# Kernel tuning notes

Measured on AMD Instinct MI355X. Metric: run time of the kernel, lower is better.

Reference implementation:

```python
import jax, jax.numpy as jnp
import numpy as np

N_K = 20000; N_E = 50000; N_U = 100000; EMB = 128
E_UND = 200000; E_EK = 400000; E_EU = 600000


def _gat(h, W, a, src, dst, n):
    """RCD GraphLayer: single-head GAT with edge softmax over incoming edges."""
    z = h @ W                                  # [N, d]
    d = z.shape[1]
    el = z @ a[:d]                             # src contribution to attn logit
    er = z @ a[d:]                             # dst contribution
    e = jax.nn.leaky_relu(el[src] + er[dst], 0.01)   # [E]
    m = jax.ops.segment_max(e, dst, num_segments=n)
    m = jnp.where(jnp.isfinite(m), m, 0.0)     # guard zero-degree nodes
    ex = jnp.exp(e - m[dst])
    s = jax.ops.segment_sum(ex, dst, num_segments=n)
    alpha = ex / s[dst]                        # per-dst softmax weights [E]
    return jax.ops.segment_sum(alpha[:, None] * z[src], dst, num_segments=n)


def setup_inputs() -> dict:
    key = jax.random.key(0)
    ks = jax.random.split(key, 32)
    sc = 1.0 / np.sqrt(EMB)
    inp = {
        'kn_emb': jax.random.normal(ks[0], (N_K, EMB), jnp.float32),
        'exer_emb': jax.random.normal(ks[1], (N_E, EMB), jnp.float32),
        'all_stu_emb': jax.random.normal(ks[2], (N_U, EMB), jnp.float32),
        'und_src': jax.random.randint(ks[3], (E_UND,), 0, N_K),
        'und_dst': jax.random.randint(ks[4], (E_UND,), 0, N_K),
        'ek_src': jax.random.randint(ks[5], (E_EK,), 0, N_E),
        'ek_dst': jax.random.randint(ks[6], (E_EK,), 0, N_K),
        'eu_src': jax.random.randint(ks[7], (E_EU,), 0, N_E),
        'eu_dst': jax.random.randint(ks[8], (E_EU,), 0, N_U),
        'W_und': jax.random.normal(ks[9], (EMB, EMB), jnp.float32) * sc,
        'a_und': jax.random.normal(ks[10], (2 * EMB,), jnp.float32) * sc,
        'W_ek': jax.random.normal(ks[11], (EMB, EMB), jnp.float32) * sc,
        'a_ek': jax.random.normal(ks[12], (2 * EMB,), jnp.float32) * sc,
        'W_ke': jax.random.normal(ks[13], (EMB, EMB), jnp.float32) * sc,
        'a_ke': jax.random.normal(ks[14], (2 * EMB,), jnp.float32) * sc,
        'W_eu': jax.random.normal(ks[15], (EMB, EMB), jnp.float32) * sc,
        'a_eu': jax.random.normal(ks[16], (2 * EMB,), jnp.float32) * sc,
        'W_ue': jax.random.normal(ks[17], (EMB, EMB), jnp.float32) * sc,
        'a_ue': jax.random.normal(ks[18], (2 * EMB,), jnp.float32) * sc,
        'k_fc2_w': jax.random.normal(ks[19], (2 * EMB,), jnp.float32) * sc,
        'k_fc2_b': jnp.zeros((1,), jnp.float32),
        'k_fc3_w': jax.random.normal(ks[20], (2 * EMB,), jnp.float32) * sc,
        'k_fc3_b': jnp.zeros((1,), jnp.float32),
        'e_fc1_w': jax.random.normal(ks[21], (2 * EMB,), jnp.float32) * sc,
        'e_fc1_b': jnp.zeros((1,), jnp.float32),
        'e_fc2_w': jax.random.normal(ks[22], (2 * EMB,), jnp.float32) * sc,
        'e_fc2_b': jnp.zeros((1,), jnp.float32),
    }
    return inp


def reference(kn_emb, exer_emb, all_stu_emb, und_src, und_dst, ek_src, ek_dst,
              eu_src, eu_dst, W_und, a_und, W_ek, a_ek, W_ke, a_ke, W_eu, a_eu,
              W_ue, a_ue, k_fc2_w, k_fc2_b, k_fc3_w, k_fc3_b, e_fc1_w, e_fc1_b,
              e_fc2_w, e_fc2_b):
    d = EMB
    # 1) undirected GAT on knowledge graph
    k_und = _gat(kn_emb, W_und, a_und, und_src, und_dst, N_K)
    # 2) exercise<->knowledge graphs on concatenated [exer; kn] nodes
    ek_nodes = jnp.concatenate([exer_emb, kn_emb], axis=0)
    e2k = _gat(ek_nodes, W_ek, a_ek, ek_src, ek_dst + N_E, N_E + N_K)
    k2e = _gat(ek_nodes, W_ke, a_ke, ek_dst + N_E, ek_src, N_E + N_K)
    # 3) exercise<->student graphs on concatenated [exer; stu] nodes
    eu_nodes = jnp.concatenate([exer_emb, all_stu_emb], axis=0)
    e2u = _gat(eu_nodes, W_eu, a_eu, eu_src, eu_dst + N_E, N_E + N_U)
    u2e = _gat(eu_nodes, W_ue, a_ue, eu_dst + N_E, eu_src, N_E + N_U)
    # knowledge fusion: attention-weighted residual combination
    A = kn_emb; C = k_und; D = e2k[N_E:]
    s2 = A @ k_fc2_w[:d] + C @ k_fc2_w[d:] + k_fc2_b[0]
    s3 = A @ k_fc3_w[:d] + D @ k_fc3_w[d:] + k_fc3_b[0]
    sk = jax.nn.softmax(jnp.stack([s2, s3], axis=1), axis=1)
    kn_out = A + sk[:, 0:1] * C + sk[:, 1:2] * D
    # exercise fusion
    Ae = exer_emb; B = k2e[:N_E]; Ce = u2e[:N_E]
    s1 = Ae @ e_fc1_w[:d] + B @ e_fc1_w[d:] + e_fc1_b[0]
    s2e = Ae @ e_fc2_w[:d] + Ce @ e_fc2_w[d:] + e_fc2_b[0]
    se = jax.nn.softmax(jnp.stack([s1, s2e], axis=1), axis=1)
    exer_out = Ae + se[:, 0:1] * B + se[:, 1:2] * Ce
    # student residual
    stu_out = all_stu_emb + e2u[N_E:]
    return (kn_out, exer_out, stu_out)
```

## Files before the change

### kernel.cpp

```cpp
#include <hip/hip_runtime.h>

#define N_K 20000
#define N_E 50000
#define N_U 100000
#define E_TOT 2200000
#define N_TOT 240000
#define PB1 0
#define PB2 20032
#define PB3 40064
#define PB4 90112
#define PB5 190144
#define PTOT 240192
#define KB1 0
#define KB2 20000
#define KB3 40000
#define KB4 90000
#define KB5 190000
#define NBKT 726
#define EPB 8192
#define NBLKA 269
#define APAD 272

typedef unsigned short u16;
typedef unsigned int u32;
typedef __bf16 bf16x8 __attribute__((ext_vector_type(8)));
typedef float f32x4 __attribute__((ext_vector_type(4)));

__device__ __forceinline__ float bf2f(u16 v){
    union { u32 u; float f; } x; x.u = ((u32)v) << 16; return x.f;
}
__device__ __forceinline__ u16 f2bf(float f){
    union { float f; u32 u; } x; x.f = f;
    u32 r = x.u + 0x7FFFu + ((x.u >> 16) & 1u);
    return (u16)(r >> 16);
}
__device__ __forceinline__ float leaky_exp(float x){
    x = x >= 0.f ? x : 0.01f*x;
    return __expf(x);
}

__device__ __forceinline__ int bucket_of(int key){
    if (key < 20000)  return key >> 8;
    if (key < 40000)  return 79  + ((key - 20000) >> 7);
    if (key < 90000)  return 236 + ((key - 40000) >> 9);
    if (key < 190000) return 334 + ((key - 90000) >> 9);
    return 530 + ((key - 190000) >> 8);
}
__device__ __forceinline__ void bucket_info(int b, int& kb, int& w, int& r){
    if (b < 79){       r=0; kb = b << 8;                 w = min(256, 20000  - kb); }
    else if (b < 236){ r=1; kb = 20000 + ((b-79)  << 7); w = min(128, 40000  - kb); }
    else if (b < 334){ r=2; kb = 40000 + ((b-236) << 9); w = min(512, 90000  - kb); }
    else if (b < 530){ r=3; kb = 90000 + ((b-334) << 9); w = min(512, 190000 - kb); }
    else {             r=4; kb = 190000 + ((b-530) << 8); w = min(256, 240000 - kb); }
}
__device__ __forceinline__ int edge_key(int e,
    const int* ud, const int* es, const int* ed, const int* vs, const int* vd){
    if (e < 200000)  return ud[e];
    if (e < 600000)  return 20000  + ed[e-200000];
    if (e < 1000000) return 40000  + es[e-600000];
    if (e < 1600000) return 90000  + vd[e-1000000];
    return 190000 + vs[e-1600000];
}
__device__ __forceinline__ int edge_src(int e,
    const int* us, const int* es, const int* ed, const int* vs, const int* vd){
    if (e < 200000)  return us[e];
    if (e < 600000)  return es[e-200000];
    if (e < 1000000) return ed[e-600000];
    if (e < 1600000) return vs[e-1000000];
    return vd[e-1600000];
}

__global__ __launch_bounds__(256) void prep_w(
    const float* W0, const float* W1, const float* W2, const float* W3, const float* W4,
    const float* a0, const float* a1, const float* a2, const float* a3, const float* a4,
    float* __restrict__ vecs, u16* __restrict__ Wf)
{
    int bid = blockIdx.x;
    if (bid < 320){
        int o = bid*4 + (threadIdx.x >> 6);
        int lane = threadIdx.x & 63;
        int which = o / 640, rem = o - which*640, g = rem >> 7, k = rem & 127;
        const float* W = g==0?W0:g==1?W1:g==2?W2:g==3?W3:W4;
        const float* a = g==0?a0:g==1?a1:g==2?a2:g==3?a3:a4;
        const float* av = a + which*128;
        int c = lane*2;
        float s = W[k*128 + c]*av[c] + W[k*128 + c + 1]*av[c+1];
        #pragma unroll
        for (int m = 32; m; m >>= 1) s += __shfl_xor(s, m);
        if (lane == 0) vecs[(which*5 + g)*128 + k] = s;
    } else {
        int t = (bid - 320)*256 + threadIdx.x;
        int g = t / 2048, i = t - g*2048;
        const float* W = g==0?W0:g==1?W1:g==2?W2:g==3?W3:W4;
        int lane = i & 63, tt = i >> 6, ks = tt & 3, ct = tt >> 2;
        int kbase = ks*32 + (lane>>4)*8;
        int c = ct*16 + (lane&15);
        #pragma unroll
        for (int j = 0; j < 8; ++j)
            Wf[g*16384 + i*8 + j] = f2bf(W[(kbase+j)*128 + c]);
    }
}

template<int ND, int WBF>
__global__ __launch_bounds__(256) void conv_dot(const float* __restrict__ h, u16* __restrict__ hb,
    const float* __restrict__ v0, const float* __restrict__ v1,
    const float* __restrict__ v2, const float* __restrict__ v3,
    float* __restrict__ o0, float* __restrict__ o1,
    float* __restrict__ o2, float* __restrict__ o3, int nrows)
{
    int w = (int)((blockIdx.x*(u32)blockDim.x + threadIdx.x) >> 6);
    int lane = threadIdx.x & 63;
    if (w >= nrows) return;
    float2 hv = *(const float2*)(h + (size_t)w*128 + lane*2);
    if (WBF)
        *(u32*)(hb + (size_t)w*128 + lane*2) = (u32)f2bf(hv.x) | ((u32)f2bf(hv.y) << 16);
    int c = lane*2;
    float d0 = hv.x*v0[c] + hv.y*v0[c+1];
    float d1 = hv.x*v1[c] + hv.y*v1[c+1];
    float d2 = 0.f, d3 = 0.f;
    if (ND == 4){
        d2 = hv.x*v2[c] + hv.y*v2[c+1];
        d3 = hv.x*v3[c] + hv.y*v3[c+1];
    }
    #pragma unroll
    for (int o = 32; o; o >>= 1){
        d0 += __shfl_xor(d0, o); d1 += __shfl_xor(d1, o);
        if (ND == 4){ d2 += __shfl_xor(d2, o); d3 += __shfl_xor(d3, o); }
    }
    if (lane == 0){
        o0[w] = d0; o1[w] = d1;
        if (ND == 4){ o2[w] = d2; o3[w] = d3; }
    }
}

__global__ __launch_bounds__(256) void bkt_hist(
    const int* __restrict__ ud, const int* __restrict__ es, const int* __restrict__ ed,
    const int* __restrict__ vs, const int* __restrict__ vd, int* __restrict__ hist)
{
    __shared__ int h[NBKT];
    for (int i = threadIdx.x; i < NBKT; i += 256) h[i] = 0;
    __syncthreads();
    int base = blockIdx.x * EPB;
    #pragma unroll 4
    for (int it = 0; it < EPB/256; ++it){
        int e = base + it*256 + threadIdx.x;
        if (e < E_TOT){
            int key = edge_key(e, ud, es, ed, vs, vd);
            atomicAdd(&h[bucket_of(key)], 1);
        }
    }
    __syncthreads();
    for (int i = threadIdx.x; i < NBKT; i += 256)
        hist[i*APAD + blockIdx.x] = h[i];
}

__global__ __launch_bounds__(512) void bkt_scan1(int* __restrict__ hist, int* __restrict__ btot)
{
    __shared__ int sm[512];
    int t = threadIdx.x;
    int v = (t < NBLKA) ? hist[blockIdx.x*APAD + t] : 0;
    sm[t] = v; __syncthreads();
    #pragma unroll
    for (int d = 1; d < 512; d <<= 1){
        int x = (t >= d) ? sm[t-d] : 0;
        __syncthreads();
        sm[t] += x;
        __syncthreads();
    }
    if (t < NBLKA) hist[blockIdx.x*APAD + t] = sm[t] - v;
    if (t == 511) btot[blockIdx.x] = sm[511];
}

__global__ __launch_bounds__(1024) void bkt_scan2(const int* __restrict__ btot, int* __restrict__ bbase)
{
    __shared__ int sm[1024];
    int t = threadIdx.x;
    int v = (t < NBKT) ? btot[t] : 0;
    sm[t] = v; __syncthreads();
    #pragma unroll
    for (int d = 1; d < 1024; d <<= 1){
        int x = (t >= d) ? sm[t-d] : 0;
        __syncthreads();
        sm[t] += x;
        __syncthreads();
    }
    if (t < NBKT) bbase[t] = sm[t] - v;
}

__global__ __launch_bounds__(256) void bkt_scatter(
    const int* __restrict__ us, const int* __restrict__ ud,
    const int* __restrict__ es, const int* __restrict__ ed,
    const int* __restrict__ vs, const int* __restrict__ vd,
    const int* __restrict__ hist, const int* __restrict__ bbase,
    uint2* __restrict__ rec)
{
    __shared__ int cur[NBKT];
    for (int i = threadIdx.x; i < NBKT; i += 256)
        cur[i] = bbase[i] + hist[i*APAD + blockIdx.x];
    __syncthreads();
    int base = blockIdx.x * EPB;
    #pragma unroll 4
    for (int it = 0; it < EPB/256; ++it){
        int e = base + it*256 + threadIdx.x;
        if (e < E_TOT){
            int key = edge_key(e, ud, es, ed, vs, vd);
            int src = edge_src(e, us, es, ed, vs, vd);
            int pos = atomicAdd(&cur[bucket_of(key)], 1);
            rec[pos] = make_uint2((u32)src, (u32)key);
        }
    }
}

__global__ __launch_bounds__(256) void bkt_cnt(const uint2* __restrict__ rec,
    const int* __restrict__ bbase, const int* __restrict__ btot, int* __restrict__ cnt)
{
    __shared__ int h[512];
    int b = blockIdx.x;
    int kb, w, r;
    bucket_info(b, kb, w, r);
    for (int i = threadIdx.x; i < 512; i += 256) h[i] = 0;
    __syncthreads();
    int start = bbase[b], n = btot[b];
    for (int i = threadIdx.x; i < n; i += 256)
        atomicAdd(&h[(int)rec[start+i].y - kb], 1);
    __syncthreads();
    for (int i = threadIdx.x; i < w; i += 256)
        cnt[kb + i] = h[i];
}

__global__ void scan1(const int* __restrict__ cnt, int* __restrict__ off, int* __restrict__ bsum, int n){
    __shared__ int sm[256];
    int t = threadIdx.x;
    int i = blockIdx.x*256 + t;
    int v = (i < n) ? cnt[i] : 0;
    sm[t] = v; __syncthreads();
    #pragma unroll
    for (int d = 1; d < 256; d <<= 1){
        int x = (t >= d) ? sm[t-d] : 0;
        __syncthreads();
        sm[t] += x;
        __syncthreads();
    }
    if (i < n) off[i] = sm[t] - v;
    if (t == 255) bsum[blockIdx.x] = sm[255];
}
__global__ void scan2(int* __restrict__ bsum, int nb){
    __shared__ int sm[1024];
    int t = threadIdx.x;
    int v = (t < nb) ? bsum[t] : 0;
    sm[t] = v; __syncthreads();
    #pragma unroll
    for (int d = 1; d < 1024; d <<= 1){
        int x = (t >= d) ? sm[t-d] : 0;
        __syncthreads();
        sm[t] += x;
        __syncthreads();
    }
    if (t < nb) bsum[t] = sm[t] - v;
}
__global__ void scan3(int* __restrict__ off, const int* __restrict__ bsum, int n){
    int i = blockIdx.x*256 + threadIdx.x;
    if (i < n) off[i] += bsum[blockIdx.x];
}

__global__ __launch_bounds__(256) void bkt_fill(const uint2* __restrict__ rec,
    const int* __restrict__ bbase, const int* __restrict__ btot,
    const int* __restrict__ offA, const float* __restrict__ erc,
    const float* __restrict__ el1, const float* __restrict__ el2,
    const float* __restrict__ el3, const float* __restrict__ el4,
    const float* __restrict__ el5, int2* __restrict__ sorted2)
{
    __shared__ int curk[512];
    __shared__ float ercs[512];
    int b = blockIdx.x;
    int kb, w, r;
    bucket_info(b, kb, w, r);
    for (int i = threadIdx.x; i < w; i += 256){
        curk[i] = offA[kb + i];
        ercs[i] = erc[kb + i];
    }
    __syncthreads();
    const float* el = r==0?el1 : r==1?el2 : r==2?el3 : r==3?el4 : el5;
    int start = bbase[b], n = btot[b];
    for (int i = threadIdx.x; i < n; i += 256){
        uint2 rc = rec[start + i];
        int local = (int)rc.y - kb;
        float ev = leaky_exp(el[rc.x] + ercs[local]);
        int pos = atomicAdd(&curk[local], 1);
        sorted2[pos] = make_int2((int)rc.x, __float_as_int(ev));
    }
}

template<int BF>
__global__ __launch_bounds__(256) void aggregate_all(
    const int* __restrict__ cnt, const int* __restrict__ off, const int2* __restrict__ sorted2,
    const void* __restrict__ hk, const void* __restrict__ he, const void* __restrict__ hs,
    u16* __restrict__ agg)
{
    int row = (int)((blockIdx.x*(u32)blockDim.x + threadIdx.x) >> 6);
    int lane = threadIdx.x & 63;
    if (row >= PTOT) return;
    int local, nb, sn;
    const void* h;
    if (row < PB2){ local=row;      nb=KB1; sn=N_K; h=hk; }
    else if (row < PB3){ local=row-PB2; nb=KB2; sn=N_K; h=he; }
    else if (row < PB4){ local=row-PB3; nb=KB3; sn=N_E; h=hk; }
    else if (row < PB5){ local=row-PB4; nb=KB4; sn=N_U; h=he; }
    else {              local=row-PB5; nb=KB5; sn=N_E; h=hs; }
    if (local >= sn) return;
    int ci = nb + local;
    int deg = cnt[ci], start = off[ci];
    float a0 = 0.f, a1 = 0.f, ssum = 0.f;
    const u32* hb32 = (const u32*)h;
    const float2* hf2 = (const float2*)h;
    int i = 0;
    for (; i + 8 <= deg; i += 8){
        int2 w[8];
        #pragma unroll
        for (int j = 0; j < 8; ++j) w[j] = sorted2[start+i+j];
        if (BF){
            u32 hv[8];
            #pragma unroll
            for (int j = 0; j < 8; ++j) hv[j] = hb32[(size_t)w[j].x*64 + lane];
            #pragma unroll
            for (int j = 0; j < 8; ++j){
                float ev = __int_as_float(w[j].y);
                a0 = fmaf(ev, bf2f((u16)hv[j]), a0);
                a1 = fmaf(ev, bf2f((u16)(hv[j]>>16)), a1);
                ssum += ev;
            }
        } else {
            float2 hv[8];
            #pragma unroll
            for (int j = 0; j < 8; ++j) hv[j] = hf2[(size_t)w[j].x*64 + lane];
            #pragma unroll
            for (int j = 0; j < 8; ++j){
                float ev = __int_as_float(w[j].y);
                a0 = fmaf(ev, hv[j].x, a0);
                a1 = fmaf(ev, hv[j].y, a1);
                ssum += ev;
            }
        }
    }
    for (; i + 4 <= deg; i += 4){
        int2 w[4];
        #pragma unroll
        for (int j = 0; j < 4; ++j) w[j] = sorted2[start+i+j];
        if (BF){
            u32 hv[4];
            #pragma unroll
            for (int j = 0; j < 4; ++j) hv[j] = hb32[(size_t)w[j].x*64 + lane];
            #pragma unroll
            for (int j = 0; j < 4; ++j){
                float ev = __int_as_float(w[j].y);
                a0 = fmaf(ev, bf2f((u16)hv[j]), a0);
                a1 = fmaf(ev, bf2f((u16)(hv[j]>>16)), a1);
                ssum += ev;
            }
        } else {
            float2 hv[4];
            #pragma unroll
            for (int j = 0; j < 4; ++j) hv[j] = hf2[(size_t)w[j].x*64 + lane];
            #pragma unroll
            for (int j = 0; j < 4; ++j){
                float ev = __int_as_float(w[j].y);
                a0 = fmaf(ev, hv[j].x, a0);
                a1 = fmaf(ev, hv[j].y, a1);
                ssum += ev;
            }
        }
    }
    for (; i < deg; ++i){
        int2 w = sorted2[start + i];
        float ev = __int_as_float(w.y);
        float x0, x1;
        if (BF){
            u32 hv = hb32[(size_t)w.x*64 + lane];
            x0 = bf2f((u16)hv); x1 = bf2f((u16)(hv>>16));
        } else {
            float2 hv = hf2[(size_t)w.x*64 + lane];
            x0 = hv.x; x1 = hv.y;
        }
        a0 = fmaf(ev, x0, a0);
        a1 = fmaf(ev, x1, a1);
        ssum += ev;
    }
    float inv = (ssum > 0.f) ? 1.f/ssum : 0.f;
    *(u32*)(agg + (size_t)row*128 + lane*2) = (u32)f2bf(a0*inv) | ((u32)f2bf(a1*inv) << 16);
}

#define KBLK 313
#define EBLK 782
#define SBLK 1563
template<int BF>
__global__ __launch_bounds__(256) void gemm_epi(const u16* __restrict__ agg, const u16* __restrict__ Wf,
    const void* __restrict__ knA, const void* __restrict__ exerA, const void* __restrict__ stuA,
    const float* __restrict__ kfc2w, const float* __restrict__ kfc2b,
    const float* __restrict__ kfc3w, const float* __restrict__ kfc3b,
    const float* __restrict__ efc1w, const float* __restrict__ efc1b,
    const float* __restrict__ efc2w, const float* __restrict__ efc2b,
    float* __restrict__ out)
{
    int wave = threadIdx.x >> 6, lane = threadIdx.x & 63;
    int bid = blockIdx.x;
    int kind, r0, sn, baseC, baseD;
    const u16 *wc, *wd;
    const void *A;
    const float *w2, *b2, *w3, *b3;
    float* outp;
    if (bid < KBLK){
        kind=0; r0=bid*64; sn=N_K; baseC=PB1; baseD=PB2;
        wc=Wf; wd=Wf+16384; A=knA; w2=kfc2w; b2=kfc2b; w3=kfc3w; b3=kfc3b; outp=out;
    } else if (bid < KBLK+EBLK){
        kind=0; r0=(bid-KBLK)*64; sn=N_E; baseC=PB3; baseD=PB5;
        wc=Wf+2*16384; wd=Wf+4*16384; A=exerA; w2=efc1w; b2=efc1b; w3=efc2w; b3=efc2b;
        outp=out + (size_t)N_K*128;
    } else {
        kind=1; r0=(bid-KBLK-EBLK)*64; sn=N_U; baseC=PB4; baseD=PB4;
        wc=Wf+3*16384; wd=nullptr; A=stuA; w2=nullptr; b2=nullptr; w3=nullptr; b3=nullptr;
        outp=out + (size_t)(N_K+N_E)*128;
    }
    int lrow = r0 + wave*16;
    if (lrow >= sn) return;
    int colb = lane & 15;
    int rlo  = (lane>>4)*4;
    const float* Af = (const float*)A;
    const u16*   Ab = (const u16*)A;

    f32x4 accC[8];
    #pragma unroll
    for (int ct = 0; ct < 8; ++ct) accC[ct] = (f32x4){0.f,0.f,0.f,0.f};
    {
        const u16* ap = agg + (size_t)(baseC + lrow + colb)*128 + ((lane>>4)*8);
        bf16x8 af[4];
        #pragma unroll
        for (int ks = 0; ks < 4; ++ks) af[ks] = *(const bf16x8*)(ap + ks*32);
        #pragma unroll
        for (int ks = 0; ks < 4; ++ks)
            #pragma unroll
            for (int ct = 0; ct < 8; ++ct){
                bf16x8 b = *(const bf16x8*)(wc + ((size_t)((ct*4+ks)*64 + lane))*8);
                accC[ct] = __builtin_amdgcn_mfma_f32_16x16x32_bf16(af[ks], b, accC[ct], 0, 0, 0);
            }
    }

    if (kind == 1){
        #pragma unroll
        for (int ct = 0; ct < 8; ++ct)
            #pragma unroll
            for (int j = 0; j < 4; ++j){
                size_t idx = (size_t)(lrow + rlo + j)*128 + ct*16 + colb;
                float av = BF ? bf2f(Ab[idx]) : Af[idx];
                outp[idx] = accC[ct][j] + av;
            }
        return;
    }

    f32x4 accD[8];
    #pragma unroll
    for (int ct = 0; ct < 8; ++ct) accD[ct] = (f32x4){0.f,0.f,0.f,0.f};
    {
        const u16* ap = agg + (size_t)(baseD + lrow + colb)*128 + ((lane>>4)*8);
        bf16x8 af[4];
        #pragma unroll
        for (int ks = 0; ks < 4; ++ks) af[ks] = *(const bf16x8*)(ap + ks*32);
        #pragma unroll
        for (int ks = 0; ks < 4; ++ks)
            #pragma unroll
            for (int ct = 0; ct < 8; ++ct){
                bf16x8 b = *(const bf16x8*)(wd + ((size_t)((ct*4+ks)*64 + lane))*8);
                accD[ct] = __builtin_amdgcn_mfma_f32_16x16x32_bf16(af[ks], b, accD[ct], 0, 0, 0);
            }
    }

    float w2l[8], w2h[8], w3l[8], w3h[8];
    #pragma unroll
    for (int ct = 0; ct < 8; ++ct){
        int c = ct*16 + colb;
        w2l[ct] = w2[c]; w2h[ct] = w2[128+c];
        w3l[ct] = w3[c]; w3h[ct] = w3[128+c];
    }
    float aA[8][4];
    #pragma unroll
    for (int ct = 0; ct < 8; ++ct)
        #pragma unroll
        for (int j = 0; j < 4; ++j){
            size_t idx = (size_t)(lrow + rlo + j)*128 + ct*16 + colb;
            aA[ct][j] = BF ? bf2f(Ab[idx]) : Af[idx];
        }
    float s2p[4] = {0.f,0.f,0.f,0.f}, s3p[4] = {0.f,0.f,0.f,0.f};
    #pragma unroll
    for (int ct = 0; ct < 8; ++ct)
        #pragma unroll
        for (int j = 0; j < 4; ++j){
            s2p[j] = fmaf(aA[ct][j], w2l[ct], fmaf(accC[ct][j], w2h[ct], s2p[j]));
            s3p[j] = fmaf(aA[ct][j], w3l[ct], fmaf(accD[ct][j], w3h[ct], s3p[j]));
        }
    #pragma unroll
    for (int m = 8; m; m >>= 1)
        #pragma unroll
        for (int j = 0; j < 4; ++j){
            s2p[j] += __shfl_xor(s2p[j], m);
            s3p[j] += __shfl_xor(s3p[j], m);
        }
    float bb2 = b2[0], bb3 = b3[0];
    #pragma unroll
    for (int j = 0; j < 4; ++j){
        float s2 = s2p[j] + bb2, s3 = s3p[j] + bb3;
        float mx = fmaxf(s2, s3);
        float e2 = __expf(s2 - mx), e3 = __expf(s3 - mx);
        float inv = 1.f/(e2 + e3);
        float p2 = e2*inv, p3 = e3*inv;
        #pragma unroll
        for (int ct = 0; ct < 8; ++ct){
            size_t idx = (size_t)(lrow + rlo + j)*128 + ct*16 + colb;
            outp[idx] = aA[ct][j] + p2*accC[ct][j] + p3*accD[ct][j];
        }
    }
}

extern "C" void kernel_launch(void* const* d_in, const int* in_sizes, int n_in,
                              void* d_out, int out_size, void* d_ws, size_t ws_size,
                              hipStream_t stream)
{
    (void)in_sizes; (void)n_in; (void)out_size;
    const float* kn   = (const float*)d_in[0];
    const float* exer = (const float*)d_in[1];
    const float* stu  = (const float*)d_in[2];
    const int* und_src = (const int*)d_in[3];
    const int* und_dst = (const int*)d_in[4];
    const int* ek_src  = (const int*)d_in[5];
    const int* ek_dst  = (const int*)d_in[6];
    const int* eu_src  = (const int*)d_in[7];
    const int* eu_dst  = (const int*)d_in[8];
    const float* W_und = (const float*)d_in[9];  const float* a_und = (const float*)d_in[10];
    const float* W_ek  = (const float*)d_in[11]; const float* a_ek  = (const float*)d_in[12];
    const float* W_ke  = (const float*)d_in[13]; const float* a_ke  = (const float*)d_in[14];
    const float* W_eu  = (const float*)d_in[15]; const float* a_eu  = (const float*)d_in[16];
    const float* W_ue  = (const float*)d_in[17]; const float* a_ue  = (const float*)d_in[18];
    const float* kfc2w = (const float*)d_in[19]; const float* kfc2b = (const float*)d_in[20];
    const float* kfc3w = (const float*)d_in[21]; const float* kfc3b = (const float*)d_in[22];
    const float* efc1w = (const float*)d_in[23]; const float* efc1b = (const float*)d_in[24];
    const float* efc2w = (const float*)d_in[25]; const float* efc2b = (const float*)d_in[26];

    char* base = (char*)d_ws;
    size_t off_b = 0;
    auto alloc = [&](size_t bytes)->char*{
        char* p = base + off_b;
        off_b += (bytes + 255) & ~(size_t)255;
        return p;
    };
    float* vecs = (float*)alloc(1280*4);
    u16*   Wf   = (u16*)  alloc(5*16384*2);
    float* el1 = (float*)alloc(N_K*4);
    float* el2 = (float*)alloc(N_E*4);
    float* el3 = (float*)alloc(N_K*4);
    float* el4 = (float*)alloc(N_E*4);
    float* el5 = (float*)alloc(N_U*4);
    float* erc = (float*)alloc((size_t)N_TOT*4);
    int* cnt  = (int*)alloc((size_t)N_TOT*4);
    int* offA = (int*)alloc((size_t)N_TOT*4);
    int* bsum = (int*)alloc(1024*4);
    int* btot = (int*)alloc(NBKT*4);
    int* bbase= (int*)alloc(NBKT*4);
    int2* sorted2 = (int2*)alloc((size_t)E_TOT*8);
    char* ublock = alloc((size_t)PTOT*128*2);
    uint2* rec = (uint2*)ublock;
    int* hist  = (int*)(ublock + (size_t)E_TOT*8);
    u16* agg   = (u16*)ublock;
    u16* knb   = (u16*)alloc((size_t)N_K*128*2);
    u16* exerb = (u16*)alloc((size_t)N_E*128*2);
    u16* stub  = (u16*)alloc((size_t)N_U*128*2);
    size_t need_bf = off_b;
    bool useBF = (ws_size >= need_bf);
    float* out = (float*)d_out;

    const int NBLK = (N_TOT + 255)/256;

    prep_w<<<360,256,0,stream>>>(W_und,W_ek,W_ke,W_eu,W_ue, a_und,a_ek,a_ke,a_eu,a_ue, vecs, Wf);

    if (useBF){
        conv_dot<4,1><<<(N_K+3)/4,256,0,stream>>>(kn,   knb,   vecs+0,    vecs+640, vecs+768,  vecs+256,  el1, erc+KB1, erc+KB2, el3, N_K);
        conv_dot<4,1><<<(N_E+3)/4,256,0,stream>>>(exer, exerb, vecs+128,  vecs+896, vecs+384,  vecs+1152, el2, erc+KB3, el4, erc+KB5, N_E);
        conv_dot<2,1><<<(N_U+3)/4,256,0,stream>>>(stu,  stub,  vecs+1024, vecs+512, nullptr, nullptr, erc+KB4, el5, nullptr, nullptr, N_U);
    } else {
        conv_dot<4,0><<<(N_K+3)/4,256,0,stream>>>(kn,   nullptr, vecs+0,    vecs+640, vecs+768,  vecs+256,  el1, erc+KB1, erc+KB2, el3, N_K);
        conv_dot<4,0><<<(N_E+3)/4,256,0,stream>>>(exer, nullptr, vecs+128,  vecs+896, vecs+384,  vecs+1152, el2, erc+KB3, el4, erc+KB5, N_E);
        conv_dot<2,0><<<(N_U+3)/4,256,0,stream>>>(stu,  nullptr, vecs+1024, vecs+512, nullptr, nullptr, erc+KB4, el5, nullptr, nullptr, N_U);
    }

    bkt_hist<<<NBLKA,256,0,stream>>>(und_dst, ek_src, ek_dst, eu_src, eu_dst, hist);
    bkt_scan1<<<NBKT,512,0,stream>>>(hist, btot);
    bkt_scan2<<<1,1024,0,stream>>>(btot, bbase);
    bkt_scatter<<<NBLKA,256,0,stream>>>(und_src, und_dst, ek_src, ek_dst, eu_src, eu_dst,
                                        hist, bbase, rec);
    bkt_cnt<<<NBKT,256,0,stream>>>(rec, bbase, btot, cnt);
    scan1<<<NBLK,256,0,stream>>>(cnt, offA, bsum, N_TOT);
    scan2<<<1,1024,0,stream>>>(bsum, NBLK);
    scan3<<<NBLK,256,0,stream>>>(offA, bsum, N_TOT);
    bkt_fill<<<NBKT,256,0,stream>>>(rec, bbase, btot, offA, erc,
                                    el1, el2, el3, el4, el5, sorted2);

    if (useBF){
        aggregate_all<1><<<(PTOT+3)/4,256,0,stream>>>(cnt, offA, sorted2, knb, exerb, stub, agg);
        gemm_epi<1><<<KBLK+EBLK+SBLK,256,0,stream>>>(agg, Wf, knb, exerb, stub,
                                                     kfc2w,kfc2b,kfc3w,kfc3b,
                                                     efc1w,efc1b,efc2w,efc2b, out);
    } else {
        aggregate_all<0><<<(PTOT+3)/4,256,0,stream>>>(cnt, offA, sorted2, kn, exer, stu, agg);
        gemm_epi<0><<<KBLK+EBLK+SBLK,256,0,stream>>>(agg, Wf, kn, exer, stu,
                                                     kfc2w,kfc2b,kfc3w,kfc3b,
                                                     efc1w,efc1b,efc2w,efc2b, out);
    }
}
```

Measured before the change: 308.7 us.

## Fuse bucket count/scan/fill and fuse aggregation into GEMM epilogue

Merges the three conv_dot launches into one conv_all kernel. Replaces bkt_cnt, the three-pass global scan and bkt_fill with a single per-bucket finalize kernel. That kernel computes counts, a local offset scan and the softmax denominators, and writes normalized alpha. It also fuses the neighbor aggregation into the GEMM/epilogue kernel, staging aggregated rows in LDS, which removes the bf16 agg intermediate and its global round trip. The cost is that each block now handles 16 nodes with serial per-wave aggregation loops, plus extra shared atomics and float atomicAdd in LDS.

```diff
diff --git a/kernel.cpp b/kernel.cpp
--- a/kernel.cpp
+++ b/kernel.cpp
@@ -5,12 +5,6 @@
 #define N_U 100000
 #define E_TOT 2200000
 #define N_TOT 240000
-#define PB1 0
-#define PB2 20032
-#define PB3 40064
-#define PB4 90112
-#define PB5 190144
-#define PTOT 240192
 #define KB1 0
 #define KB2 20000
 #define KB3 40000
@@ -20,6 +14,9 @@
 #define EPB 8192
 #define NBLKA 269
 #define APAD 272
+#define KN_B 1250
+#define EX_B 3125
+#define ST_B 6250
 
 typedef unsigned short u16;
 typedef unsigned int u32;
@@ -101,35 +98,49 @@
     }
 }
 
-template<int ND, int WBF>
-__global__ __launch_bounds__(256) void conv_dot(const float* __restrict__ h, u16* __restrict__ hb,
-    const float* __restrict__ v0, const float* __restrict__ v1,
-    const float* __restrict__ v2, const float* __restrict__ v3,
-    float* __restrict__ o0, float* __restrict__ o1,
-    float* __restrict__ o2, float* __restrict__ o3, int nrows)
+template<int WBF>
+__global__ __launch_bounds__(256) void conv_all(
+    const float* __restrict__ kn, const float* __restrict__ exer, const float* __restrict__ stu,
+    u16* __restrict__ knb, u16* __restrict__ exerb, u16* __restrict__ stub,
+    const float* __restrict__ vecs,
+    float* __restrict__ el1, float* __restrict__ el2, float* __restrict__ el3,
+    float* __restrict__ el4, float* __restrict__ el5, float* __restrict__ erc)
 {
     int w = (int)((blockIdx.x*(u32)blockDim.x + threadIdx.x) >> 6);
     int lane = threadIdx.x & 63;
-    if (w >= nrows) return;
-    float2 hv = *(const float2*)(h + (size_t)w*128 + lane*2);
+    if (w >= 170000) return;
+    const float* h; u16* hb; int local, nd;
+    const float *v0,*v1,*v2,*v3;
+    float *o0,*o1,*o2,*o3;
+    if (w < 20000){
+        local = w; h = kn; hb = knb; nd = 4;
+        v0=vecs+0;    v1=vecs+640;  v2=vecs+768;  v3=vecs+256;
+        o0=el1; o1=erc+KB1; o2=erc+KB2; o3=el3;
+    } else if (w < 70000){
+        local = w - 20000; h = exer; hb = exerb; nd = 4;
+        v0=vecs+128;  v1=vecs+896;  v2=vecs+384;  v3=vecs+1152;
+        o0=el2; o1=erc+KB3; o2=el4; o3=erc+KB5;
+    } else {
+        local = w - 70000; h = stu; hb = stub; nd = 2;
+        v0=vecs+1024; v1=vecs+512;  v2=vecs;      v3=vecs;
+        o0=erc+KB4; o1=el5; o2=nullptr; o3=nullptr;
+    }
+    float2 hv = *(const float2*)(h + (size_t)local*128 + lane*2);
     if (WBF)
-        *(u32*)(hb + (size_t)w*128 + lane*2) = (u32)f2bf(hv.x) | ((u32)f2bf(hv.y) << 16);
+        *(u32*)(hb + (size_t)local*128 + lane*2) = (u32)f2bf(hv.x) | ((u32)f2bf(hv.y) << 16);
     int c = lane*2;
     float d0 = hv.x*v0[c] + hv.y*v0[c+1];
     float d1 = hv.x*v1[c] + hv.y*v1[c+1];
-    float d2 = 0.f, d3 = 0.f;
-    if (ND == 4){
-        d2 = hv.x*v2[c] + hv.y*v2[c+1];
-        d3 = hv.x*v3[c] + hv.y*v3[c+1];
-    }
+    float d2 = hv.x*v2[c] + hv.y*v2[c+1];
+    float d3 = hv.x*v3[c] + hv.y*v3[c+1];
     #pragma unroll
     for (int o = 32; o; o >>= 1){
         d0 += __shfl_xor(d0, o); d1 += __shfl_xor(d1, o);
-        if (ND == 4){ d2 += __shfl_xor(d2, o); d3 += __shfl_xor(d3, o); }
+        d2 += __shfl_xor(d2, o); d3 += __shfl_xor(d3, o);
     }
     if (lane == 0){
-        o0[w] = d0; o1[w] = d1;
-        if (ND == 4){ o2[w] = d2; o3[w] = d3; }
+        o0[local] = d0; o1[local] = d1;
+        if (nd == 4){ o2[local] = d2; o3[local] = d3; }
     }
 }
 
@@ -211,291 +222,249 @@
     }
 }
 
-__global__ __launch_bounds__(256) void bkt_cnt(const uint2* __restrict__ rec,
-    const int* __restrict__ bbase, const int* __restrict__ btot, int* __restrict__ cnt)
-{
-    __shared__ int h[512];
-    int b = blockIdx.x;
+__global__ __launch_bounds__(512) void bkt_finalize(const uint2* __restrict__ rec,
+    const int* __restrict__ bbase, const int* __restrict__ btot,
+    const float* __restrict__ erc,
+    const float* __restrict__ el1, const float* __restrict__ el2,
+    const float* __restrict__ el3, const float* __restrict__ el4,
+    const float* __restrict__ el5,
+    int* __restrict__ cnt, int* __restrict__ offA, int2* __restrict__ sorted2)
+{
+    __shared__ int   h[512];
+    __shared__ float s[512];
+    __shared__ float ercs[512];
+    __shared__ int   sm[512];
+    __shared__ int   curk[512];
+    int b = blockIdx.x, t = threadIdx.x;
     int kb, w, r;
     bucket_info(b, kb, w, r);
-    for (int i = threadIdx.x; i < 512; i += 256) h[i] = 0;
-    __syncthreads();
+    h[t] = 0; s[t] = 0.f;
+    if (t < w) ercs[t] = erc[kb + t];
+    __syncthreads();
+    const float* el = r==0?el1 : r==1?el2 : r==2?el3 : r==3?el4 : el5;
     int start = bbase[b], n = btot[b];
-    for (int i = threadIdx.x; i < n; i += 256)
-        atomicAdd(&h[(int)rec[start+i].y - kb], 1);
-    __syncthreads();
-    for (int i = threadIdx.x; i < w; i += 256)
-        cnt[kb + i] = h[i];
-}
-
-__global__ void scan1(const int* __restrict__ cnt, int* __restrict__ off, int* __restrict__ bsum, int n){
-    __shared__ int sm[256];
-    int t = threadIdx.x;
-    int i = blockIdx.x*256 + t;
-    int v = (i < n) ? cnt[i] : 0;
-    sm[t] = v; __syncthreads();
-    #pragma unroll
-    for (int d = 1; d < 256; d <<= 1){
+    for (int i = t; i < n; i += 512){
+        uint2 rc = rec[start + i];
+        int local = (int)rc.y - kb;
+        atomicAdd(&h[local], 1);
+        atomicAdd(&s[local], leaky_exp(el[rc.x] + ercs[local]));
+    }
+    __syncthreads();
+    int hv = h[t];
+    if (t < w) cnt[kb + t] = hv;
+    sm[t] = hv; __syncthreads();
+    #pragma unroll
+    for (int d = 1; d < 512; d <<= 1){
         int x = (t >= d) ? sm[t-d] : 0;
         __syncthreads();
         sm[t] += x;
         __syncthreads();
     }
-    if (i < n) off[i] = sm[t] - v;
-    if (t == 255) bsum[blockIdx.x] = sm[255];
-}
-__global__ void scan2(int* __restrict__ bsum, int nb){
-    __shared__ int sm[1024];
-    int t = threadIdx.x;
-    int v = (t < nb) ? bsum[t] : 0;
-    sm[t] = v; __syncthreads();
-    #pragma unroll
-    for (int d = 1; d < 1024; d <<= 1){
-        int x = (t >= d) ? sm[t-d] : 0;
-        __syncthreads();
-        sm[t] += x;
-        __syncthreads();
-    }
-    if (t < nb) bsum[t] = sm[t] - v;
-}
-__global__ void scan3(int* __restrict__ off, const int* __restrict__ bsum, int n){
-    int i = blockIdx.x*256 + threadIdx.x;
-    if (i < n) off[i] += bsum[blockIdx.x];
-}
-
-__global__ __launch_bounds__(256) void bkt_fill(const uint2* __restrict__ rec,
-    const int* __restrict__ bbase, const int* __restrict__ btot,
-    const int* __restrict__ offA, const float* __restrict__ erc,
-    const float* __restrict__ el1, const float* __restrict__ el2,
-    const float* __restrict__ el3, const float* __restrict__ el4,
-    const float* __restrict__ el5, int2* __restrict__ sorted2)
-{
-    __shared__ int curk[512];
-    __shared__ float ercs[512];
-    int b = blockIdx.x;
-    int kb, w, r;
-    bucket_info(b, kb, w, r);
-    for (int i = threadIdx.x; i < w; i += 256){
-        curk[i] = offA[kb + i];
-        ercs[i] = erc[kb + i];
-    }
-    __syncthreads();
-    const float* el = r==0?el1 : r==1?el2 : r==2?el3 : r==3?el4 : el5;
-    int start = bbase[b], n = btot[b];
-    for (int i = threadIdx.x; i < n; i += 256){
+    int pos0 = start + sm[t] - hv;
+    if (t < w) offA[kb + t] = pos0;
+    curk[t] = pos0;
+    __syncthreads();
+    for (int i = t; i < n; i += 512){
         uint2 rc = rec[start + i];
         int local = (int)rc.y - kb;
-        float ev = leaky_exp(el[rc.x] + ercs[local]);
+        float alpha = leaky_exp(el[rc.x] + ercs[local]) / s[local];
         int pos = atomicAdd(&curk[local], 1);
-        sorted2[pos] = make_int2((int)rc.x, __float_as_int(ev));
+        sorted2[pos] = make_int2((int)rc.x, __float_as_int(alpha));
     }
 }
 
 template<int BF>
-__global__ __launch_bounds__(256) void aggregate_all(
-    const int* __restrict__ cnt, const int* __restrict__ off, const int2* __restrict__ sorted2,
+__global__ __launch_bounds__(256) void agg_gemm_epi(
+    const int* __restrict__ cnt, const int* __restrict__ offA, const int2* __restrict__ sorted2,
     const void* __restrict__ hk, const void* __restrict__ he, const void* __restrict__ hs,
-    u16* __restrict__ agg)
-{
-    int row = (int)((blockIdx.x*(u32)blockDim.x + threadIdx.x) >> 6);
-    int lane = threadIdx.x & 63;
-    if (row >= PTOT) return;
-    int local, nb, sn;
-    const void* h;
-    if (row < PB2){ local=row;      nb=KB1; sn=N_K; h=hk; }
-    else if (row < PB3){ local=row-PB2; nb=KB2; sn=N_K; h=he; }
-    else if (row < PB4){ local=row-PB3; nb=KB3; sn=N_E; h=hk; }
-    else if (row < PB5){ local=row-PB4; nb=KB4; sn=N_U; h=he; }
-    else {              local=row-PB5; nb=KB5; sn=N_E; h=hs; }
-    if (local >= sn) return;
-    int ci = nb + local;
-    int deg = cnt[ci], start = off[ci];
-    float a0 = 0.f, a1 = 0.f, ssum = 0.f;
-    const u32* hb32 = (const u32*)h;
-    const float2* hf2 = (const float2*)h;
-    int i = 0;
-    for (; i + 8 <= deg; i += 8){
-        int2 w[8];
-        #pragma unroll
-        for (int j = 0; j < 8; ++j) w[j] = sorted2[start+i+j];
-        if (BF){
-            u32 hv[8];
-            #pragma unroll
-            for (int j = 0; j < 8; ++j) hv[j] = hb32[(size_t)w[j].x*64 + lane];
-            #pragma unroll
-            for (int j = 0; j < 8; ++j){
-                float ev = __int_as_float(w[j].y);
-                a0 = fmaf(ev, bf2f((u16)hv[j]), a0);
-                a1 = fmaf(ev, bf2f((u16)(hv[j]>>16)), a1);
-                ssum += ev;
-            }
-        } else {
-            float2 hv[8];
-            #pragma unroll
-            for (int j = 0; j < 8; ++j) hv[j] = hf2[(size_t)w[j].x*64 + lane];
-            #pragma unroll
-            for (int j = 0; j < 8; ++j){
-                float ev = __int_as_float(w[j].y);
-                a0 = fmaf(ev, hv[j].x, a0);
-                a1 = fmaf(ev, hv[j].y, a1);
-                ssum += ev;
-            }
-        }
-    }
-    for (; i + 4 <= deg; i += 4){
-        int2 w[4];
-        #pragma unroll
-        for (int j = 0; j < 4; ++j) w[j] = sorted2[start+i+j];
-        if (BF){
-            u32 hv[4];
-            #pragma unroll
-            for (int j = 0; j < 4; ++j) hv[j] = hb32[(size_t)w[j].x*64 + lane];
-            #pragma unroll
-            for (int j = 0; j < 4; ++j){
-                float ev = __int_as_float(w[j].y);
-                a0 = fmaf(ev, bf2f((u16)hv[j]), a0);
-                a1 = fmaf(ev, bf2f((u16)(hv[j]>>16)), a1);
-                ssum += ev;
-            }
-        } else {
-            float2 hv[4];
-            #pragma unroll
-            for (int j = 0; j < 4; ++j) hv[j] = hf2[(size_t)w[j].x*64 + lane];
-            #pragma unroll
-            for (int j = 0; j < 4; ++j){
-                float ev = __int_as_float(w[j].y);
-                a0 = fmaf(ev, hv[j].x, a0);
-                a1 = fmaf(ev, hv[j].y, a1);
-                ssum += ev;
-            }
-        }
-    }
-    for (; i < deg; ++i){
-        int2 w = sorted2[start + i];
-        float ev = __int_as_float(w.y);
-        float x0, x1;
-        if (BF){
-            u32 hv = hb32[(size_t)w.x*64 + lane];
-            x0 = bf2f((u16)hv); x1 = bf2f((u16)(hv>>16));
-        } else {
-            float2 hv = hf2[(size_t)w.x*64 + lane];
-            x0 = hv.x; x1 = hv.y;
-        }
-        a0 = fmaf(ev, x0, a0);
-        a1 = fmaf(ev, x1, a1);
-        ssum += ev;
-    }
-    float inv = (ssum > 0.f) ? 1.f/ssum : 0.f;
-    *(u32*)(agg + (size_t)row*128 + lane*2) = (u32)f2bf(a0*inv) | ((u32)f2bf(a1*inv) << 16);
-}
-
-#define KBLK 313
-#define EBLK 782
-#define SBLK 1563
-template<int BF>
-__global__ __launch_bounds__(256) void gemm_epi(const u16* __restrict__ agg, const u16* __restrict__ Wf,
-    const void* __restrict__ knA, const void* __restrict__ exerA, const void* __restrict__ stuA,
+    const u16* __restrict__ Wf,
     const float* __restrict__ kfc2w, const float* __restrict__ kfc2b,
     const float* __restrict__ kfc3w, const float* __restrict__ kfc3b,
     const float* __restrict__ efc1w, const float* __restrict__ efc1b,
     const float* __restrict__ efc2w, const float* __restrict__ efc2b,
     float* __restrict__ out)
 {
+    __shared__ u16 ldsC[16*136];
+    __shared__ u16 ldsD[16*136];
+    __shared__ float sred2[16], sred3[16], p2s[16], p3s[16];
+
+    int bid = blockIdx.x;
     int wave = threadIdx.x >> 6, lane = threadIdx.x & 63;
-    int bid = blockIdx.x;
-    int kind, r0, sn, baseC, baseD;
+    int kind, node0, keyC, keyD;
+    const void *hC, *hD, *Aseg;
     const u16 *wc, *wd;
-    const void *A;
     const float *w2, *b2, *w3, *b3;
     float* outp;
-    if (bid < KBLK){
-        kind=0; r0=bid*64; sn=N_K; baseC=PB1; baseD=PB2;
-        wc=Wf; wd=Wf+16384; A=knA; w2=kfc2w; b2=kfc2b; w3=kfc3w; b3=kfc3b; outp=out;
-    } else if (bid < KBLK+EBLK){
-        kind=0; r0=(bid-KBLK)*64; sn=N_E; baseC=PB3; baseD=PB5;
-        wc=Wf+2*16384; wd=Wf+4*16384; A=exerA; w2=efc1w; b2=efc1b; w3=efc2w; b3=efc2b;
-        outp=out + (size_t)N_K*128;
+    if (bid < KN_B){
+        kind=0; node0 = bid*16;
+        keyC = KB1 + node0; keyD = KB2 + node0;
+        hC = hk; hD = he; Aseg = hk;
+        wc = Wf; wd = Wf + 16384;
+        w2=kfc2w; b2=kfc2b; w3=kfc3w; b3=kfc3b;
+        outp = out;
+    } else if (bid < KN_B + EX_B){
+        kind=0; node0 = (bid - KN_B)*16;
+        keyC = KB3 + node0; keyD = KB5 + node0;
+        hC = hk; hD = hs; Aseg = he;
+        wc = Wf + 2*16384; wd = Wf + 4*16384;
+        w2=efc1w; b2=efc1b; w3=efc2w; b3=efc2b;
+        outp = out + (size_t)N_K*128;
     } else {
-        kind=1; r0=(bid-KBLK-EBLK)*64; sn=N_U; baseC=PB4; baseD=PB4;
-        wc=Wf+3*16384; wd=nullptr; A=stuA; w2=nullptr; b2=nullptr; w3=nullptr; b3=nullptr;
-        outp=out + (size_t)(N_K+N_E)*128;
-    }
-    int lrow = r0 + wave*16;
-    if (lrow >= sn) return;
-    int colb = lane & 15;
-    int rlo  = (lane>>4)*4;
-    const float* Af = (const float*)A;
-    const u16*   Ab = (const u16*)A;
-
-    f32x4 accC[8];
-    #pragma unroll
-    for (int ct = 0; ct < 8; ++ct) accC[ct] = (f32x4){0.f,0.f,0.f,0.f};
-    {
-        const u16* ap = agg + (size_t)(baseC + lrow + colb)*128 + ((lane>>4)*8);
-        bf16x8 af[4];
-        #pragma unroll
-        for (int ks = 0; ks < 4; ++ks) af[ks] = *(const bf16x8*)(ap + ks*32);
-        #pragma unroll
-        for (int ks = 0; ks < 4; ++ks)
+        kind=1; node0 = (bid - KN_B - EX_B)*16;
+        keyC = KB4 + node0; keyD = 0;
+        hC = he; hD = nullptr; Aseg = hs;
+        wc = Wf + 3*16384; wd = nullptr;
+        w2=nullptr; b2=nullptr; w3=nullptr; b3=nullptr;
+        outp = out + (size_t)(N_K + N_E)*128;
+    }
+
+    int rpw = (kind == 0) ? 8 : 4;
+    for (int rr = 0; rr < rpw; ++rr){
+        int c = wave*rpw + rr;
+        int seg = c >> 4, nd = c & 15;
+        int key = (seg == 0 ? keyC : keyD) + nd;
+        const u32* hb32 = (const u32*)(seg == 0 ? hC : hD);
+        const float2* hf2 = (const float2*)(seg == 0 ? hC : hD);
+        int deg = cnt[key], start = offA[key];
+        float a0 = 0.f, a1 = 0.f;
+        int i = 0;
+        for (; i + 8 <= deg; i += 8){
+            int2 w[8];
             #pragma unroll
-            for (int ct = 0; ct < 8; ++ct){
-                bf16x8 b = *(const bf16x8*)(wc + ((size_t)((ct*4+ks)*64 + lane))*8);
-                accC[ct] = __builtin_amdgcn_mfma_f32_16x16x32_bf16(af[ks], b, accC[ct], 0, 0, 0);
+            for (int j = 0; j < 8; ++j) w[j] = sorted2[start+i+j];
+            if (BF){
+                u32 hv[8];
+                #pragma unroll
+                for (int j = 0; j < 8; ++j) hv[j] = hb32[(size_t)w[j].x*64 + lane];
+                #pragma unroll
+                for (int j = 0; j < 8; ++j){
+                    float al = __int_as_float(w[j].y);
+                    a0 = fmaf(al, bf2f((u16)hv[j]), a0);
+                    a1 = fmaf(al, bf2f((u16)(hv[j]>>16)), a1);
+                }
+            } else {
+                float2 hv[8];
+                #pragma unroll
+                for (int j = 0; j < 8; ++j) hv[j] = hf2[(size_t)w[j].x*64 + lane];
+                #pragma unroll
+                for (int j = 0; j < 8; ++j){
+                    float al = __int_as_float(w[j].y);
+                    a0 = fmaf(al, hv[j].x, a0);
+                    a1 = fmaf(al, hv[j].y, a1);
+                }
             }
+        }
+        for (; i + 4 <= deg; i += 4){
+            int2 w[4];
+            #pragma unroll
+            for (int j = 0; j < 4; ++j) w[j] = sorted2[start+i+j];
+            if (BF){
+                u32 hv[4];
+                #pragma unroll
+                for (int j = 0; j < 4; ++j) hv[j] = hb32[(size_t)w[j].x*64 + lane];
+                #pragma unroll
+                for (int j = 0; j < 4; ++j){
+                    float al = __int_as_float(w[j].y);
+                    a0 = fmaf(al, bf2f((u16)hv[j]), a0);
+                    a1 = fmaf(al, bf2f((u16)(hv[j]>>16)), a1);
+                }
+            } else {
+                float2 hv[4];
+                #pragma unroll
+                for (int j = 0; j < 4; ++j) hv[j] = hf2[(size_t)w[j].x*64 + lane];
+                #pragma unroll
+                for (int j = 0; j < 4; ++j){
+                    float al = __int_as_float(w[j].y);
+                    a0 = fmaf(al, hv[j].x, a0);
+                    a1 = fmaf(al, hv[j].y, a1);
+                }
+            }
+        }
+        for (; i < deg; ++i){
+            int2 w = sorted2[start + i];
+            float al = __int_as_float(w.y);
+            if (BF){
+                u32 hv = hb32[(size_t)w.x*64 + lane];
+                a0 = fmaf(al, bf2f((u16)hv), a0);
+                a1 = fmaf(al, bf2f((u16)(hv>>16)), a1);
+            } else {
+                float2 hv = hf2[(size_t)w.x*64 + lane];
+                a0 = fmaf(al, hv.x, a0);
+                a1 = fmaf(al, hv.y, a1);
+            }
+        }
+        u16* dstl = (seg == 0 ? ldsC : ldsD) + nd*136 + lane*2;
+        *(u32*)dstl = (u32)f2bf(a0) | ((u32)f2bf(a1) << 16);
+    }
+    if (threadIdx.x < 16){ sred2[threadIdx.x] = 0.f; sred3[threadIdx.x] = 0.f; }
+    __syncthreads();
+
+    int colb = lane & 15, rlo = (lane >> 4)*4;
+    const float* Af = (const float*)Aseg;
+    const u16*   Ab = (const u16*)Aseg;
+
+    bf16x8 afC[4];
+    #pragma unroll
+    for (int ks = 0; ks < 4; ++ks)
+        afC[ks] = *(const bf16x8*)(ldsC + (lane & 15)*136 + ks*32 + (lane >> 4)*8);
+    f32x4 accC[2];
+    accC[0] = (f32x4){0.f,0.f,0.f,0.f}; accC[1] = (f32x4){0.f,0.f,0.f,0.f};
+    #pragma unroll
+    for (int ci = 0; ci < 2; ++ci){
+        int ct = wave*2 + ci;
+        #pragma unroll
+        for (int ks = 0; ks < 4; ++ks){
+            bf16x8 bfr = *(const bf16x8*)(wc + ((ct*4+ks)*64 + lane)*8);
+            accC[ci] = __builtin_amdgcn_mfma_f32_16x16x32_bf16(afC[ks], bfr, accC[ci], 0, 0, 0);
+        }
     }
 
     if (kind == 1){
         #pragma unroll
-        for (int ct = 0; ct < 8; ++ct)
+        for (int ci = 0; ci < 2; ++ci){
+            int ct = wave*2 + ci;
             #pragma unroll
             for (int j = 0; j < 4; ++j){
-                size_t idx = (size_t)(lrow + rlo + j)*128 + ct*16 + colb;
+                size_t idx = (size_t)(node0 + rlo + j)*128 + ct*16 + colb;
                 float av = BF ? bf2f(Ab[idx]) : Af[idx];
-                outp[idx] = accC[ct][j] + av;
+                outp[idx] = accC[ci][j] + av;
             }
+        }
         return;
     }
 
-    f32x4 accD[8];
-    #pragma unroll
-    for (int ct = 0; ct < 8; ++ct) accD[ct] = (f32x4){0.f,0.f,0.f,0.f};
-    {
-        const u16* ap = agg + (size_t)(baseD + lrow + colb)*128 + ((lane>>4)*8);
-        bf16x8 af[4];
-        #pragma unroll
-        for (int ks = 0; ks < 4; ++ks) af[ks] = *(const bf16x8*)(ap + ks*32);
-        #pragma unroll
-        for (int ks = 0; ks < 4; ++ks)
-            #pragma unroll
-            for (int ct = 0; ct < 8; ++ct){
-                bf16x8 b = *(const bf16x8*)(wd + ((size_t)((ct*4+ks)*64 + lane))*8);
-                accD[ct] = __builtin_amdgcn_mfma_f32_16x16x32_bf16(af[ks], b, accD[ct], 0, 0, 0);
-            }
-    }
-
-    float w2l[8], w2h[8], w3l[8], w3h[8];
-    #pragma unroll
-    for (int ct = 0; ct < 8; ++ct){
-        int c = ct*16 + colb;
-        w2l[ct] = w2[c]; w2h[ct] = w2[128+c];
-        w3l[ct] = w3[c]; w3h[ct] = w3[128+c];
-    }
-    float aA[8][4];
-    #pragma unroll
-    for (int ct = 0; ct < 8; ++ct)
+    bf16x8 afD[4];
+    #pragma unroll
+    for (int ks = 0; ks < 4; ++ks)
+        afD[ks] = *(const bf16x8*)(ldsD + (lane & 15)*136 + ks*32 + (lane >> 4)*8);
+    f32x4 accD[2];
+    accD[0] = (f32x4){0.f,0.f,0.f,0.f}; accD[1] = (f32x4){0.f,0.f,0.f,0.f};
+    #pragma unroll
+    for (int ci = 0; ci < 2; ++ci){
+        int ct = wave*2 + ci;
+        #pragma unroll
+        for (int ks = 0; ks < 4; ++ks){
+            bf16x8 bfr = *(const bf16x8*)(wd + ((ct*4+ks)*64 + lane)*8);
+            accD[ci] = __builtin_amdgcn_mfma_f32_16x16x32_bf16(afD[ks], bfr, accD[ci], 0, 0, 0);
+        }
+    }
+
+    float aA[2][4];
+    float s2p[4] = {0.f,0.f,0.f,0.f}, s3p[4] = {0.f,0.f,0.f,0.f};
+    #pragma unroll
+    for (int ci = 0; ci < 2; ++ci){
+        int ct = wave*2 + ci;
+        float w2l = w2[ct*16 + colb], w2h = w2[128 + ct*16 + colb];
+        float w3l = w3[ct*16 + colb], w3h = w3[128 + ct*16 + colb];
         #pragma unroll
         for (int j = 0; j < 4; ++j){
-            size_t idx = (size_t)(lrow + rlo + j)*128 + ct*16 + colb;
-            aA[ct][j] = BF ? bf2f(Ab[idx]) : Af[idx];
-        }
-    float s2p[4] = {0.f,0.f,0.f,0.f}, s3p[4] = {0.f,0.f,0.f,0.f};
-    #pragma unroll
-    for (int ct = 0; ct < 8; ++ct)
-        #pragma unroll
-        for (int j = 0; j < 4; ++j){
-            s2p[j] = fmaf(aA[ct][j], w2l[ct], fmaf(accC[ct][j], w2h[ct], s2p[j]));
-            s3p[j] = fmaf(aA[ct][j], w3l[ct], fmaf(accD[ct][j], w3h[ct], s3p[j]));
-        }
+            size_t idx = (size_t)(node0 + rlo + j)*128 + ct*16 + colb;
+            float av = BF ? bf2f(Ab[idx]) : Af[idx];
+            aA[ci][j] = av;
+            s2p[j] = fmaf(av, w2l, fmaf(accC[ci][j], w2h, s2p[j]));
+            s3p[j] = fmaf(av, w3l, fmaf(accD[ci][j], w3h, s3p[j]));
+        }
+    }
     #pragma unroll
     for (int m = 8; m; m >>= 1)
         #pragma unroll
@@ -503,18 +472,32 @@
             s2p[j] += __shfl_xor(s2p[j], m);
             s3p[j] += __shfl_xor(s3p[j], m);
         }
-    float bb2 = b2[0], bb3 = b3[0];
-    #pragma unroll
-    for (int j = 0; j < 4; ++j){
-        float s2 = s2p[j] + bb2, s3 = s3p[j] + bb3;
+    if (colb == 0){
+        #pragma unroll
+        for (int j = 0; j < 4; ++j){
+            atomicAdd(&sred2[rlo + j], s2p[j]);
+            atomicAdd(&sred3[rlo + j], s3p[j]);
+        }
+    }
+    __syncthreads();
+    if (threadIdx.x < 16){
+        float s2 = sred2[threadIdx.x] + b2[0];
+        float s3 = sred3[threadIdx.x] + b3[0];
         float mx = fmaxf(s2, s3);
         float e2 = __expf(s2 - mx), e3 = __expf(s3 - mx);
         float inv = 1.f/(e2 + e3);
-        float p2 = e2*inv, p3 = e3*inv;
-        #pragma unroll
-        for (int ct = 0; ct < 8; ++ct){
-            size_t idx = (size_t)(lrow + rlo + j)*128 + ct*16 + colb;
-            outp[idx] = aA[ct][j] + p2*accC[ct][j] + p3*accD[ct][j];
+        p2s[threadIdx.x] = e2*inv;
+        p3s[threadIdx.x] = e3*inv;
+    }
+    __syncthreads();
+    #pragma unroll
+    for (int ci = 0; ci < 2; ++ci){
+        int ct = wave*2 + ci;
+        #pragma unroll
+        for (int j = 0; j < 4; ++j){
+            int row = rlo + j;
+            size_t idx = (size_t)(node0 + row)*128 + ct*16 + colb;
+            outp[idx] = aA[ci][j] + p2s[row]*accC[ci][j] + p3s[row]*accD[ci][j];
         }
     }
 }
@@ -560,14 +543,11 @@
     float* erc = (float*)alloc((size_t)N_TOT*4);
     int* cnt  = (int*)alloc((size_t)N_TOT*4);
     int* offA = (int*)alloc((size_t)N_TOT*4);
-    int* bsum = (int*)alloc(1024*4);
     int* btot = (int*)alloc(NBKT*4);
     int* bbase= (int*)alloc(NBKT*4);
+    int* hist = (int*)alloc((size_t)NBKT*APAD*4);
+    uint2* rec = (uint2*)alloc((size_t)E_TOT*8);
     int2* sorted2 = (int2*)alloc((size_t)E_TOT*8);
-    char* ublock = alloc((size_t)PTOT*128*2);
-    uint2* rec = (uint2*)ublock;
-    int* hist  = (int*)(ublock + (size_t)E_TOT*8);
-    u16* agg   = (u16*)ublock;
     u16* knb   = (u16*)alloc((size_t)N_K*128*2);
     u16* exerb = (u16*)alloc((size_t)N_E*128*2);
     u16* stub  = (u16*)alloc((size_t)N_U*128*2);
@@ -575,41 +555,31 @@
     bool useBF = (ws_size >= need_bf);
     float* out = (float*)d_out;
 
-    const int NBLK = (N_TOT + 255)/256;
-
     prep_w<<<360,256,0,stream>>>(W_und,W_ek,W_ke,W_eu,W_ue, a_und,a_ek,a_ke,a_eu,a_ue, vecs, Wf);
 
-    if (useBF){
-        conv_dot<4,1><<<(N_K+3)/4,256,0,stream>>>(kn,   knb,   vecs+0,    vecs+640, vecs+768,  vecs+256,  el1, erc+KB1, erc+KB2, el3, N_K);
-        conv_dot<4,1><<<(N_E+3)/4,256,0,stream>>>(exer, exerb, vecs+128,  vecs+896, vecs+384,  vecs+1152, el2, erc+KB3, el4, erc+KB5, N_E);
-        conv_dot<2,1><<<(N_U+3)/4,256,0,stream>>>(stu,  stub,  vecs+1024, vecs+512, nullptr, nullptr, erc+KB4, el5, nullptr, nullptr, N_U);
-    } else {
-        conv_dot<4,0><<<(N_K+3)/4,256,0,stream>>>(kn,   nullptr, vecs+0,    vecs+640, vecs+768,  vecs+256,  el1, erc+KB1, erc+KB2, el3, N_K);
-        conv_dot<4,0><<<(N_E+3)/4,256,0,stream>>>(exer, nullptr, vecs+128,  vecs+896, vecs+384,  vecs+1152, el2, erc+KB3, el4, erc+KB5, N_E);
-        conv_dot<2,0><<<(N_U+3)/4,256,0,stream>>>(stu,  nullptr, vecs+1024, vecs+512, nullptr, nullptr, erc+KB4, el5, nullptr, nullptr, N_U);
-    }
+    if (useBF)
+        conv_all<1><<<(170000+3)/4,256,0,stream>>>(kn, exer, stu, knb, exerb, stub, vecs,
+                                                   el1, el2, el3, el4, el5, erc);
+    else
+        conv_all<0><<<(170000+3)/4,256,0,stream>>>(kn, exer, stu, knb, exerb, stub, vecs,
+                                                   el1, el2, el3, el4, el5, erc);
 
     bkt_hist<<<NBLKA,256,0,stream>>>(und_dst, ek_src, ek_dst, eu_src, eu_dst, hist);
     bkt_scan1<<<NBKT,512,0,stream>>>(hist, btot);
     bkt_scan2<<<1,1024,0,stream>>>(btot, bbase);
     bkt_scatter<<<NBLKA,256,0,stream>>>(und_src, und_dst, ek_src, ek_dst, eu_src, eu_dst,
                                         hist, bbase, rec);
-    bkt_cnt<<<NBKT,256,0,stream>>>(rec, bbase, btot, cnt);
-    scan1<<<NBLK,256,0,stream>>>(cnt, offA, bsum, N_TOT);
-    scan2<<<1,1024,0,stream>>>(bsum, NBLK);
-    scan3<<<NBLK,256,0,stream>>>(offA, bsum, N_TOT);
-    bkt_fill<<<NBKT,256,0,stream>>>(rec, bbase, btot, offA, erc,
-                                    el1, el2, el3, el4, el5, sorted2);
+    bkt_finalize<<<NBKT,512,0,stream>>>(rec, bbase, btot, erc,
+                                        el1, el2, el3, el4, el5,
+                                        cnt, offA, sorted2);
 
     if (useBF){
-        aggregate_all<1><<<(PTOT+3)/4,256,0,stream>>>(cnt, offA, sorted2, knb, exerb, stub, agg);
-        gemm_epi<1><<<KBLK+EBLK+SBLK,256,0,stream>>>(agg, Wf, knb, exerb, stub,
-                                                     kfc2w,kfc2b,kfc3w,kfc3b,
-                                                     efc1w,efc1b,efc2w,efc2b, out);
+        agg_gemm_epi<1><<<KN_B+EX_B+ST_B,256,0,stream>>>(cnt, offA, sorted2,
+            knb, exerb, stub, Wf,
+            kfc2w,kfc2b,kfc3w,kfc3b, efc1w,efc1b,efc2w,efc2b, out);
     } else {
-        aggregate_all<0><<<(PTOT+3)/4,256,0,stream>>>(cnt, offA, sorted2, kn, exer, stu, agg);
-        gemm_epi<0><<<KBLK+EBLK+SBLK,256,0,stream>>>(agg, Wf, kn, exer, stu,
-                                                     kfc2w,kfc2b,kfc3w,kfc3b,
-                                                     efc1w,efc1b,efc2w,efc2b, out);
-    }
-}
+        agg_gemm_epi<0><<<KN_B+EX_B+ST_B,256,0,stream>>>(cnt, offA, sorted2,
+            kn, exer, stu, Wf,
+            kfc2w,kfc2b,kfc3w,kfc3b, efc1w,efc1b,efc2w,efc2b, out);
+    }
+}
```

Measured after the change: 308.6 us. About the same (-0.0%).
